# Performance work log

Hardware: AMD Instinct MI355X
Metric: run time of the kernel (lower is better)

Reference implementation:

```python
import jax, jax.numpy as jnp
import numpy as np

# dims (see shape_source): seq S = d_t+1 must equal d_k for the unary quantum loader
B, T, D_IN = 128, 127, 48
DK = 128
S = T + 1            # tokens incl. class token; S == DK
H, L = 8, 6
P = (S * S - S) // 2  # RBS angles per head (pyramid circuit over S wires)


def _pyramid_pairs(n):
    # deterministic pyramid ordering of n(n-1)/2 adjacent-pair Givens rotations
    a, b = [], []
    for k in range(n - 1):
        for i in range(k, -1, -1):
            a.append(i)
            b.append(i + 1)
    return np.asarray(a, np.int32), np.asarray(b, np.int32)


def _build_W(phi, pa, pb, n):
    # classical simulation of the RBS pyramid circuit restricted to the unary
    # subspace: product of Givens rotations -> orthogonal n x n matrix
    def step(W, inp):
        ia, ib, th = inp
        c, s = jnp.cos(th), jnp.sin(th)
        ra, rb = W[ia], W[ib]
        W = W.at[ia].set(c * ra - s * rb)
        W = W.at[ib].set(s * ra + c * rb)
        return W, None
    W0 = jnp.eye(n, dtype=phi.dtype)
    W, _ = jax.lax.scan(step, W0, (pa, pb, phi))
    return W


def _layer_norm(x, g, b, eps=1e-5):
    m = jnp.mean(x, axis=-1, keepdims=True)
    v = jnp.mean((x - m) ** 2, axis=-1, keepdims=True)
    return (x - m) * jax.lax.rsqrt(v + eps) * g + b


def setup_inputs() -> dict:
    key = jax.random.key(0)
    ks = jax.random.split(key, 8)
    f32 = jnp.float32
    return {
        "x": jax.random.normal(ks[0], (B, T, D_IN), f32),
        "embed_w": jax.random.normal(ks[1], (DK, D_IN), f32) / np.sqrt(D_IN),
        "embed_b": jnp.zeros((DK,), f32),
        "class_token": jax.random.normal(ks[2], (DK,), f32) / DK,
        "norm0_g": jnp.ones((DK,), f32),
        "norm0_b": jnp.zeros((DK,), f32),
        "Vw": jax.random.normal(ks[3], (L, H, DK, DK), f32) / np.sqrt(DK),
        "Vb": jnp.zeros((L, H, DK), f32),
        "ln_g": jnp.ones((L, H, DK), f32),
        "ln_b": jnp.zeros((L, H, DK), f32),
        "phi": jax.random.normal(ks[4], (L, H, P), f32) / np.sqrt(S),
        "merger_w": jax.random.normal(ks[5], (L, H), f32) / np.sqrt(H),
        "merger_b": jnp.zeros((L,), f32),
    }


def reference(x, embed_w, embed_b, class_token, norm0_g, norm0_b,
              Vw, Vb, ln_g, ln_b, phi, merger_w, merger_b):
    Bsz = x.shape[0]
    pa, pb = _pyramid_pairs(S)
    # orthogonal score matrices for every (layer, head)
    Ws = jax.vmap(lambda p: _build_W(p, pa, pb, S))(phi.reshape(L * H, P))
    Ws = Ws.reshape(L, H, S, S)

    # embed patches, prepend class token (pos_embedding add is a no-op in the
    # original source: bare `+self.pos_embedding` statement, so it is omitted)
    tok = jnp.einsum('btf,df->btd', x, embed_w) + embed_b
    h = jnp.concatenate([jnp.broadcast_to(class_token, (Bsz, 1, DK)), tok], axis=1)
    h = _layer_norm(h, norm0_g, norm0_b)

    scale = 1.0 / np.sqrt(DK)
    for l in range(L):
        nrm = jnp.sqrt(jnp.sum(h * h, axis=-1))      # input3: token norms [B,S]
        u = h / nrm[..., None]                        # unit tokens (convert_array)
        hh, nn, uu = h, nrm, u

        def head(W, vw, vb, g, be):
            V = jnp.einsum('bsd,ed->bse', hh, vw) + vb
            M = jnp.einsum('bsd,de,bte->bst', uu, W, uu)
            A = (M * M) * (nn[:, :, None] * nn[:, None, :])
            Pm = jax.nn.softmax(A * scale, axis=-1)
            return _layer_norm(jnp.einsum('bst,btd->bsd', Pm, V) + hh, g, be)

        hs = jax.vmap(head)(Ws[l], Vw[l], Vb[l], ln_g[l], ln_b[l])  # [H,B,S,D]
        h = jnp.einsum('hbsd,h->bsd', hs, merger_w[l]) + merger_b[l]
    return h[:, -1, :]
```

## Files before the change

### kernel.cpp

```cpp
#include <hip/hip_runtime.h>
#include <hip/hip_bf16.h>


typedef __bf16 bf16x8 __attribute__((ext_vector_type(8)));
typedef float  f32x4  __attribute__((ext_vector_type(4)));
typedef unsigned int u32;

__device__ __forceinline__ int sidx(int row, int col)
{
    return row * 128 + ((((col >> 3) ^ (row & 15)) << 3) | (col & 7));
}

__global__ void __launch_bounds__(256)
vw_frag_kernel(const float* __restrict__ vw, __bf16* __restrict__ cvwf)
{
    const int f    = blockIdx.x * 256 + threadIdx.x;
    const int lane = f & 63;
    const int k0   = (f >> 6) & 3;
    const int t    = (f >> 8) & 7;
    const int lh   = f >> 11;
    const int row  = t * 16 + (lane & 15);
    const int col  = k0 * 32 + (lane >> 4) * 8;

    const float* src = vw + (lh * 128 + row) * 128 + col;
    __bf16* dst = cvwf + f * 8;
#pragma unroll
    for (int j = 0; j < 8; j++) dst[j] = (__bf16)src[j];
}

__global__ void __launch_bounds__(64)
sincos_kernel(const float* __restrict__ phi, float2* __restrict__ csn)
{
    const int mat = blockIdx.x >> 8;
    const int t   = blockIdx.x & 255;
    const int j   = threadIdx.x;

    float th = 0.f;
    if (t < 253) {
        const int p = t & 1, i = 2 * j + p;
        const int lim = min(t, 252 - t);
        if (i <= lim) {
            const int k = (t + i) >> 1;
            th = phi[mat * 8128 + ((k * (k + 1)) >> 1) + (k - i)];
        }
    }
    float sn, cs;
    __sincosf(th, &sn, &cs);
    csn[(mat * 256 + t) * 64 + j] = make_float2(cs, sn);
}

__global__ void __launch_bounds__(64)
build_w_kernel(const float2* __restrict__ csn, __bf16* __restrict__ wt)
{
    const int mat = blockIdx.x >> 5;
    const int grp = blockIdx.x & 31;
    const int c0  = grp * 4;
    const int lam = threadIdx.x;

    const float2* base = csn + (mat * 256) * 64 + lam;

    float vlo[4], vhi[4];
#pragma unroll
    for (int j = 0; j < 4; j++) {
        vlo[j] = (2 * lam     == c0 + j) ? 1.f : 0.f;
        vhi[j] = (2 * lam + 1 == c0 + j) ? 1.f : 0.f;
    }

    float2 buf[3][16];
#pragma unroll
    for (int k = 0; k < 16; k++) buf[0][k] = base[k * 64];
#pragma unroll
    for (int k = 0; k < 16; k++) buf[1][k] = base[(16 + k) * 64];

#pragma unroll
    for (int g = 0; g < 16; g++) {
        const int cb = g % 3;
        if (g < 14) {
            const int nb = (g + 2) % 3;
#pragma unroll
            for (int k = 0; k < 16; k++)
                buf[nb][k] = base[((g + 2) * 16 + k) * 64];
        }
#pragma unroll
        for (int p = 0; p < 8; p++) {
            {
                const float cs = buf[cb][2 * p].x, sn = buf[cb][2 * p].y;
#pragma unroll
                for (int j = 0; j < 4; j++) {
                    float lo = vlo[j], hi = vhi[j];
                    vlo[j] = cs * lo - sn * hi;
                    vhi[j] = sn * lo + cs * hi;
                }
            }
            {
                const float cs = buf[cb][2 * p + 1].x, sn = buf[cb][2 * p + 1].y;
#pragma unroll
                for (int j = 0; j < 4; j++) {
                    float y  = __shfl_down(vlo[j], 1);
                    float x  = vhi[j];
                    float xn = cs * x - sn * y;
                    float yn = sn * x + cs * y;
                    vhi[j] = xn;
                    float z = __shfl_up(yn, 1);
                    if (lam > 0) vlo[j] = z;
                }
            }
        }
    }

    u32* wtu = (u32*)wt;
#pragma unroll
    for (int j = 0; j < 4; j++) {
        __bf16 va = (__bf16)vlo[j];
        __bf16 vb = (__bf16)vhi[j];
        u32 pk = (u32)__builtin_bit_cast(unsigned short, va)
               | ((u32)__builtin_bit_cast(unsigned short, vb) << 16);
        wtu[mat * 8192 + (c0 + j) * 64 + lam] = pk;
    }
}

static __device__ __forceinline__ float block_sum_128(float v, float* sred)
{
#pragma unroll
    for (int m = 32; m; m >>= 1) v += __shfl_xor(v, m);
    __syncthreads();
    if ((threadIdx.x & 63) == 0) sred[threadIdx.x >> 6] = v;
    __syncthreads();
    return sred[0] + sred[1];
}

__global__ void __launch_bounds__(128)
embed_kernel(const float* __restrict__ x,  const float* __restrict__ ew,
             const float* __restrict__ eb, const float* __restrict__ ct,
             const float* __restrict__ g0, const float* __restrict__ b0,
             float* __restrict__ hf, __bf16* __restrict__ hb, float* __restrict__ invn)
{
    __shared__ float sx[48];
    __shared__ float sred[2];
    const int b = blockIdx.x & 127, s = blockIdx.x >> 7, d = threadIdx.x;

    float val;
    if (s == 0) {
        val = ct[d];
    } else {
        if (d < 48) sx[d] = x[(b * 127 + (s - 1)) * 48 + d];
        __syncthreads();
        float aa = 0.f;
#pragma unroll
        for (int f = 0; f < 48; f++) aa = fmaf(sx[f], ew[d * 48 + f], aa);
        val = aa + eb[d];
    }
    float mean = block_sum_128(val, sred) * (1.f / 128.f);
    float xc   = val - mean;
    float var  = block_sum_128(xc * xc, sred) * (1.f / 128.f);
    float y    = xc * rsqrtf(var + 1e-5f) * g0[d] + b0[d];
    float ss   = block_sum_128(y * y, sred);

    const int o = (b * 128 + s) * 128 + d;
    hf[o] = y;
    hb[o] = (__bf16)y;
    if (d == 0) invn[b * 128 + s] = rsqrtf(ss);
}

__global__ void __launch_bounds__(512, 4)
attn_kernel(int l,
            const float*  __restrict__ hf,  const __bf16* __restrict__ hb,
            const float*  __restrict__ invn, const __bf16* __restrict__ wt,
            const __bf16* __restrict__ vwf, const float* __restrict__ vb,
            const float* __restrict__ lng,  const float* __restrict__ lnb,
            const float* __restrict__ mwp,  __bf16* __restrict__ hs)
{
    __shared__ __align__(16) __bf16 sH[128 * 128];
    __shared__ __align__(16) __bf16 sY[128 * 128];
    __shared__ float sInv[128];
    __shared__ float sVb[128];
    __shared__ float sLg[128];
    __shared__ float sLb[128];

    const int tid  = threadIdx.x;
    const int lane = tid & 63, w = tid >> 6;
    const int l15  = lane & 15, quad = lane >> 4;
    const int b    = blockIdx.x & 127;
    const int hh   = blockIdx.x >> 7;
    const int lh   = l * 8 + hh;

    const __bf16* hbp = hb + b * 16384;
    const __bf16* wtp = wt + lh * 16384;

#pragma unroll
    for (int c = 0; c < 4; c++) {
        int ch  = tid + c * 512;
        int row = ch >> 4, cc = ch & 15;
        bf16x8 hv = *(const bf16x8*)(hbp + ch * 8);
        bf16x8 wv = *(const bf16x8*)(wtp + ch * 8);
        *(bf16x8*)(&sH[sidx(row, cc * 8)]) = hv;
        *(bf16x8*)(&sY[sidx(row, cc * 8)]) = wv;
    }
    if (tid < 128) {
        sInv[tid] = invn[b * 128 + tid];
        sVb[tid]  = vb[lh * 128 + tid];
        sLg[tid]  = lng[lh * 128 + tid];
        sLb[tid]  = lnb[lh * 128 + tid];
    }
    __syncthreads();

    const int r0 = w * 16;
    const int kq = quad * 8;
    const int q4 = quad * 4;
    const f32x4 vzero = {0.f, 0.f, 0.f, 0.f};

    f32x4 acc[8];

    auto mmL = [&](const __bf16* Ab, const __bf16* Bb) {
#pragma unroll
        for (int t = 0; t < 8; t++) acc[t] = vzero;
#pragma unroll
        for (int k0 = 0; k0 < 128; k0 += 32) {
            const int kk = k0 + kq;
            bf16x8 a0 = *(const bf16x8*)(&Ab[sidx(r0 + l15, kk)]);
#pragma unroll
            for (int t = 0; t < 8; t++) {
                bf16x8 bb = *(const bf16x8*)(&Bb[sidx(t * 16 + l15, kk)]);
                acc[t] = __builtin_amdgcn_mfma_f32_16x16x32_bf16(a0, bb, acc[t], 0, 0, 0);
            }
        }
    };

    mmL(sH, sY);
    __syncthreads();
#pragma unroll
    for (int t = 0; t < 8; t++)
#pragma unroll
        for (int r = 0; r < 4; r++)
            sY[sidx(r0 + q4 + r, t * 16 + l15)] = (__bf16)acc[t][r];

    mmL(sY, sH);

    {
        const float scale2 = 0.08838834764831843f * 1.4426950408889634f;
        float invt[8];
#pragma unroll
        for (int t = 0; t < 8; t++) invt[t] = sInv[t * 16 + l15];
        float invs[4];
#pragma unroll
        for (int r = 0; r < 4; r++) invs[r] = sInv[r0 + q4 + r];

        float mx[4] = {-3e38f, -3e38f, -3e38f, -3e38f};
#pragma unroll
        for (int t = 0; t < 8; t++)
#pragma unroll
            for (int r = 0; r < 4; r++) {
                float g = acc[t][r];
                float v = g * g * invs[r] * invt[t] * scale2;
                acc[t][r] = v;
                mx[r] = fmaxf(mx[r], v);
            }
#pragma unroll
        for (int m = 1; m < 16; m <<= 1)
#pragma unroll
            for (int r = 0; r < 4; r++) mx[r] = fmaxf(mx[r], __shfl_xor(mx[r], m));

        float sm[4] = {0.f, 0.f, 0.f, 0.f};
#pragma unroll
        for (int t = 0; t < 8; t++)
#pragma unroll
            for (int r = 0; r < 4; r++) {
                float e = exp2f(acc[t][r] - mx[r]);
                acc[t][r] = e;
                sm[r] += e;
            }
#pragma unroll
        for (int m = 1; m < 16; m <<= 1)
#pragma unroll
            for (int r = 0; r < 4; r++) sm[r] += __shfl_xor(sm[r], m);
#pragma unroll
        for (int r = 0; r < 4; r++) sm[r] = 1.0f / sm[r];
#pragma unroll
        for (int t = 0; t < 8; t++)
#pragma unroll
            for (int r = 0; r < 4; r++)
                sY[sidx(r0 + q4 + r, t * 16 + l15)] = (__bf16)(acc[t][r] * sm[r]);
    }

    float hres[8][4];
    {
        const float* hfp = hf + (b * 128 + r0 + q4) * 128;
#pragma unroll
        for (int t = 0; t < 8; t++)
#pragma unroll
            for (int r = 0; r < 4; r++)
                hres[t][r] = hfp[r * 128 + t * 16 + l15];
    }

    {
        const __bf16* vbase = vwf + (size_t)lh * 16384;
#pragma unroll
        for (int t = 0; t < 8; t++) acc[t] = vzero;
#pragma unroll
        for (int k0c = 0; k0c < 4; k0c++) {
            const int kk = k0c * 32 + kq;
            bf16x8 a0 = *(const bf16x8*)(&sH[sidx(r0 + l15, kk)]);
#pragma unroll
            for (int t = 0; t < 8; t++) {
                bf16x8 bb = *(const bf16x8*)(vbase + ((t * 4 + k0c) * 64 + lane) * 8);
                acc[t] = __builtin_amdgcn_mfma_f32_16x16x32_bf16(a0, bb, acc[t], 0, 0, 0);
            }
        }
    }
    __syncthreads();

    {
        float vbv[8];
#pragma unroll
        for (int t = 0; t < 8; t++) vbv[t] = sVb[t * 16 + l15];
#pragma unroll
        for (int t = 0; t < 8; t++)
#pragma unroll
            for (int r = 0; r < 4; r++)
                sH[sidx(t * 16 + l15, r0 + q4 + r)] = (__bf16)(acc[t][r] + vbv[t]);
    }
    __syncthreads();

    mmL(sY, sH);

    {
        const float mw = mwp[lh];
        float lgv[8], lbv[8];
#pragma unroll
        for (int t = 0; t < 8; t++) {
            lgv[t] = sLg[t * 16 + l15];
            lbv[t] = sLb[t * 16 + l15];
        }
        float sum_[4] = {0.f, 0.f, 0.f, 0.f};
        float sq_[4]  = {0.f, 0.f, 0.f, 0.f};
#pragma unroll
        for (int t = 0; t < 8; t++)
#pragma unroll
            for (int r = 0; r < 4; r++) {
                float xx = acc[t][r] + hres[t][r];
                acc[t][r] = xx;
                sum_[r] += xx;
                sq_[r]  += xx * xx;
            }
#pragma unroll
        for (int m = 1; m < 16; m <<= 1)
#pragma unroll
            for (int r = 0; r < 4; r++) {
                sum_[r] += __shfl_xor(sum_[r], m);
                sq_[r]  += __shfl_xor(sq_[r], m);
            }
        float mean[4], rstd[4];
#pragma unroll
        for (int r = 0; r < 4; r++) {
            mean[r] = sum_[r] * (1.f / 128.f);
            float var = sq_[r] * (1.f / 128.f) - mean[r] * mean[r];
            rstd[r] = rsqrtf(fmaxf(var, 0.f) + 1e-5f);
        }
        __bf16* hsp = hs + ((hh * 128 + b) * 128 + r0 + q4) * 128;
#pragma unroll
        for (int t = 0; t < 8; t++)
#pragma unroll
            for (int r = 0; r < 4; r++) {
                float y = (acc[t][r] - mean[r]) * rstd[r] * lgv[t] + lbv[t];
                hsp[r * 128 + t * 16 + l15] = (__bf16)(y * mw);
            }
    }
}

__global__ void __launch_bounds__(128)
merge_kernel(const __bf16* __restrict__ hs, const float* __restrict__ mbp, int l,
             float* __restrict__ hf, __bf16* __restrict__ hb, float* __restrict__ invn,
             float* __restrict__ out, int last)
{
    __shared__ float sred[2];
    const int b = blockIdx.x & 127, s = blockIdx.x >> 7, d = threadIdx.x;

    float acc = mbp[l];
#pragma unroll
    for (int h = 0; h < 8; h++)
        acc += (float)hs[((h * 128 + b) * 128 + s) * 128 + d];

    float ss = block_sum_128(acc * acc, sred);

    const int o = (b * 128 + s) * 128 + d;
    hf[o] = acc;
    hb[o] = (__bf16)acc;
    if (d == 0) invn[b * 128 + s] = rsqrtf(ss);
    if (last && s == 127) out[b * 128 + d] = acc;
}

extern "C" void kernel_launch(void* const* d_in, const int* in_sizes, int n_in,
                              void* d_out, int out_size, void* d_ws, size_t ws_size,
                              hipStream_t stream)
{
    (void)in_sizes; (void)n_in; (void)out_size; (void)ws_size;

    const float* x   = (const float*)d_in[0];
    const float* ew  = (const float*)d_in[1];
    const float* eb  = (const float*)d_in[2];
    const float* ct  = (const float*)d_in[3];
    const float* g0  = (const float*)d_in[4];
    const float* b0  = (const float*)d_in[5];
    const float* vw  = (const float*)d_in[6];
    const float* vb  = (const float*)d_in[7];
    const float* lng = (const float*)d_in[8];
    const float* lnb = (const float*)d_in[9];
    const float* phi = (const float*)d_in[10];
    const float* mw  = (const float*)d_in[11];
    const float* mb  = (const float*)d_in[12];
    float* out = (float*)d_out;

    char* ws = (char*)d_ws;
    __bf16* wt   = (__bf16*)(ws);
    float*  hf   = (float*)(ws + 1572864);
    __bf16* hb   = (__bf16*)(ws + 9961472);
    float*  invn = (float*)(ws + 14155776);
    __bf16* hs   = (__bf16*)(ws + 14221312);
    __bf16* cvwf = (__bf16*)(ws + 47775744);
    float2* csn  = (float2*)(ws + 49348608);

    vw_frag_kernel<<<384, 256, 0, stream>>>(vw, cvwf);
    sincos_kernel<<<48 * 256, 64, 0, stream>>>(phi, csn);
    build_w_kernel<<<1536, 64, 0, stream>>>(csn, wt);
    embed_kernel<<<16384, 128, 0, stream>>>(x, ew, eb, ct, g0, b0, hf, hb, invn);
    for (int l = 0; l < 6; l++) {
        attn_kernel<<<1024, 512, 0, stream>>>(l, hf, hb, invn, wt, cvwf, vb,
                                              lng, lnb, mw, hs);
        merge_kernel<<<16384, 128, 0, stream>>>(hs, mb, l, hf, hb, invn, out,
                                                (l == 5) ? 1 : 0);
    }
}
```

Before: 427.1 us.

## Fuse head merge into next layer's attention load and merge prep kernels

Removes the separate merge kernel: each attention kernel now sums the 8 per-head outputs of the previous layer while loading its tile, and computes token norms in place, using ping-pong hs buffers. The sincos and Vw fragment prep kernels are merged into one launch, and the embed kernel handles 4 tokens per block and drops the norm output. This cuts launch count and the hf/hb write-then-read traffic per layer. In exchange, each of the 8 head blocks re-reads all 8 head slices, so there is redundant global reads (8x the merge read volume) and the residual is now taken from bf16 sums rather than fp32.

Result: slower. 709.2 us (+66.0%).

```diff
diff --git a/kernel.cpp b/kernel.cpp
--- a/kernel.cpp
+++ b/kernel.cpp
@@ -12,41 +12,38 @@
 }
 
 __global__ void __launch_bounds__(256)
-vw_frag_kernel(const float* __restrict__ vw, __bf16* __restrict__ cvwf)
-{
-    const int f    = blockIdx.x * 256 + threadIdx.x;
-    const int lane = f & 63;
-    const int k0   = (f >> 6) & 3;
-    const int t    = (f >> 8) & 7;
-    const int lh   = f >> 11;
-    const int row  = t * 16 + (lane & 15);
-    const int col  = k0 * 32 + (lane >> 4) * 8;
-
-    const float* src = vw + (lh * 128 + row) * 128 + col;
-    __bf16* dst = cvwf + f * 8;
-#pragma unroll
-    for (int j = 0; j < 8; j++) dst[j] = (__bf16)src[j];
-}
-
-__global__ void __launch_bounds__(64)
-sincos_kernel(const float* __restrict__ phi, float2* __restrict__ csn)
-{
-    const int mat = blockIdx.x >> 8;
-    const int t   = blockIdx.x & 255;
-    const int j   = threadIdx.x;
-
-    float th = 0.f;
-    if (t < 253) {
-        const int p = t & 1, i = 2 * j + p;
-        const int lim = min(t, 252 - t);
-        if (i <= lim) {
-            const int k = (t + i) >> 1;
-            th = phi[mat * 8128 + ((k * (k + 1)) >> 1) + (k - i)];
-        }
-    }
-    float sn, cs;
-    __sincosf(th, &sn, &cs);
-    csn[(mat * 256 + t) * 64 + j] = make_float2(cs, sn);
+prep_kernel(const float* __restrict__ phi, float2* __restrict__ csn,
+            const float* __restrict__ vw,  __bf16* __restrict__ cvwf)
+{
+    if (blockIdx.x < 3072) {
+        const int mat = blockIdx.x >> 6;
+        const int t   = ((blockIdx.x & 63) << 2) + (threadIdx.x >> 6);
+        const int j   = threadIdx.x & 63;
+        float th = 0.f;
+        if (t < 253) {
+            const int p = t & 1, i = 2 * j + p;
+            const int lim = min(t, 252 - t);
+            if (i <= lim) {
+                const int k = (t + i) >> 1;
+                th = phi[mat * 8128 + ((k * (k + 1)) >> 1) + (k - i)];
+            }
+        }
+        float sn, cs;
+        __sincosf(th, &sn, &cs);
+        csn[(mat * 256 + t) * 64 + j] = make_float2(cs, sn);
+    } else {
+        const int f    = (blockIdx.x - 3072) * 256 + threadIdx.x;
+        const int lane = f & 63;
+        const int k0   = (f >> 6) & 3;
+        const int t    = (f >> 8) & 7;
+        const int lh   = f >> 11;
+        const int row  = t * 16 + (lane & 15);
+        const int col  = k0 * 32 + (lane >> 4) * 8;
+        const float* src = vw + (lh * 128 + row) * 128 + col;
+        __bf16* dst = cvwf + f * 8;
+#pragma unroll
+        for (int j = 0; j < 8; j++) dst[j] = (__bf16)src[j];
+    }
 }
 
 __global__ void __launch_bounds__(64)
@@ -119,60 +116,63 @@
     }
 }
 
-static __device__ __forceinline__ float block_sum_128(float v, float* sred)
-{
-#pragma unroll
-    for (int m = 32; m; m >>= 1) v += __shfl_xor(v, m);
-    __syncthreads();
-    if ((threadIdx.x & 63) == 0) sred[threadIdx.x >> 6] = v;
-    __syncthreads();
-    return sred[0] + sred[1];
-}
-
-__global__ void __launch_bounds__(128)
+__global__ void __launch_bounds__(512)
 embed_kernel(const float* __restrict__ x,  const float* __restrict__ ew,
              const float* __restrict__ eb, const float* __restrict__ ct,
              const float* __restrict__ g0, const float* __restrict__ b0,
-             float* __restrict__ hf, __bf16* __restrict__ hb, float* __restrict__ invn)
-{
-    __shared__ float sx[48];
-    __shared__ float sred[2];
-    const int b = blockIdx.x & 127, s = blockIdx.x >> 7, d = threadIdx.x;
+             float* __restrict__ hf, __bf16* __restrict__ hb)
+{
+    __shared__ float sx[4][48];
+    __shared__ float sred[4][2];
+    const int d  = threadIdx.x & 127, sq = threadIdx.x >> 7;
+    const int wh = (threadIdx.x >> 6) & 1;
+    const int b  = blockIdx.x & 127;
+    const int s  = (blockIdx.x >> 7) * 4 + sq;
+
+    if (s > 0 && d < 48) sx[sq][d] = x[(b * 127 + (s - 1)) * 48 + d];
+    __syncthreads();
 
     float val;
     if (s == 0) {
         val = ct[d];
     } else {
-        if (d < 48) sx[d] = x[(b * 127 + (s - 1)) * 48 + d];
-        __syncthreads();
         float aa = 0.f;
 #pragma unroll
-        for (int f = 0; f < 48; f++) aa = fmaf(sx[f], ew[d * 48 + f], aa);
+        for (int f = 0; f < 48; f++) aa = fmaf(sx[sq][f], ew[d * 48 + f], aa);
         val = aa + eb[d];
     }
-    float mean = block_sum_128(val, sred) * (1.f / 128.f);
+    float v = val;
+#pragma unroll
+    for (int m = 32; m; m >>= 1) v += __shfl_xor(v, m);
+    if ((threadIdx.x & 63) == 0) sred[sq][wh] = v;
+    __syncthreads();
+    float mean = (sred[sq][0] + sred[sq][1]) * (1.f / 128.f);
     float xc   = val - mean;
-    float var  = block_sum_128(xc * xc, sred) * (1.f / 128.f);
-    float y    = xc * rsqrtf(var + 1e-5f) * g0[d] + b0[d];
-    float ss   = block_sum_128(y * y, sred);
+    __syncthreads();
+    v = xc * xc;
+#pragma unroll
+    for (int m = 32; m; m >>= 1) v += __shfl_xor(v, m);
+    if ((threadIdx.x & 63) == 0) sred[sq][wh] = v;
+    __syncthreads();
+    float var = (sred[sq][0] + sred[sq][1]) * (1.f / 128.f);
+    float y   = xc * rsqrtf(var + 1e-5f) * g0[d] + b0[d];
 
     const int o = (b * 128 + s) * 128 + d;
     hf[o] = y;
     hb[o] = (__bf16)y;
-    if (d == 0) invn[b * 128 + s] = rsqrtf(ss);
 }
 
 __global__ void __launch_bounds__(512, 4)
-attn_kernel(int l,
-            const float*  __restrict__ hf,  const __bf16* __restrict__ hb,
-            const float*  __restrict__ invn, const __bf16* __restrict__ wt,
-            const __bf16* __restrict__ vwf, const float* __restrict__ vb,
-            const float* __restrict__ lng,  const float* __restrict__ lnb,
-            const float* __restrict__ mwp,  __bf16* __restrict__ hs)
+attn_kernel(int l, int first,
+            const float*  __restrict__ hf,   const __bf16* __restrict__ hsrc,
+            const __bf16* __restrict__ wt,   const __bf16* __restrict__ vwf,
+            const float*  __restrict__ vb,   const float* __restrict__ lng,
+            const float*  __restrict__ lnb,  const float* __restrict__ mwp,
+            const float*  __restrict__ mbp,  __bf16* __restrict__ hs)
 {
     __shared__ __align__(16) __bf16 sH[128 * 128];
     __shared__ __align__(16) __bf16 sY[128 * 128];
-    __shared__ float sInv[128];
+    __shared__ float sInvR[128];
     __shared__ float sVb[128];
     __shared__ float sLg[128];
     __shared__ float sLb[128];
@@ -184,23 +184,44 @@
     const int hh   = blockIdx.x >> 7;
     const int lh   = l * 8 + hh;
 
-    const __bf16* hbp = hb + b * 16384;
     const __bf16* wtp = wt + lh * 16384;
+    const float mbv = first ? 0.f : mbp[l - 1];
 
 #pragma unroll
     for (int c = 0; c < 4; c++) {
         int ch  = tid + c * 512;
         int row = ch >> 4, cc = ch & 15;
-        bf16x8 hv = *(const bf16x8*)(hbp + ch * 8);
         bf16x8 wv = *(const bf16x8*)(wtp + ch * 8);
-        *(bf16x8*)(&sH[sidx(row, cc * 8)]) = hv;
+        float v[8];
+        if (first) {
+            bf16x8 hv = *(const bf16x8*)(hsrc + b * 16384 + ch * 8);
+#pragma unroll
+            for (int j = 0; j < 8; j++) v[j] = (float)hv[j];
+        } else {
+#pragma unroll
+            for (int j = 0; j < 8; j++) v[j] = mbv;
+#pragma unroll
+            for (int h8 = 0; h8 < 8; h8++) {
+                bf16x8 tv = *(const bf16x8*)(hsrc + (size_t)h8 * 2097152
+                                             + (b * 128 + row) * 128 + cc * 8);
+#pragma unroll
+                for (int j = 0; j < 8; j++) v[j] += (float)tv[j];
+            }
+        }
+        float ss = 0.f;
+        bf16x8 hv8;
+#pragma unroll
+        for (int j = 0; j < 8; j++) { ss = fmaf(v[j], v[j], ss); hv8[j] = (__bf16)v[j]; }
+        *(bf16x8*)(&sH[sidx(row, cc * 8)]) = hv8;
         *(bf16x8*)(&sY[sidx(row, cc * 8)]) = wv;
+#pragma unroll
+        for (int m = 1; m < 16; m <<= 1) ss += __shfl_xor(ss, m);
+        if ((tid & 15) == 0) sInvR[row] = ss;
     }
     if (tid < 128) {
-        sInv[tid] = invn[b * 128 + tid];
-        sVb[tid]  = vb[lh * 128 + tid];
-        sLg[tid]  = lng[lh * 128 + tid];
-        sLb[tid]  = lnb[lh * 128 + tid];
+        sVb[tid] = vb[lh * 128 + tid];
+        sLg[tid] = lng[lh * 128 + tid];
+        sLb[tid] = lnb[lh * 128 + tid];
     }
     __syncthreads();
 
@@ -240,10 +261,10 @@
         const float scale2 = 0.08838834764831843f * 1.4426950408889634f;
         float invt[8];
 #pragma unroll
-        for (int t = 0; t < 8; t++) invt[t] = sInv[t * 16 + l15];
+        for (int t = 0; t < 8; t++) invt[t] = rsqrtf(sInvR[t * 16 + l15]);
         float invs[4];
 #pragma unroll
-        for (int r = 0; r < 4; r++) invs[r] = sInv[r0 + q4 + r];
+        for (int r = 0; r < 4; r++) invs[r] = rsqrtf(sInvR[r0 + q4 + r]);
 
         float mx[4] = {-3e38f, -3e38f, -3e38f, -3e38f};
 #pragma unroll
@@ -283,13 +304,26 @@
     }
 
     float hres[8][4];
-    {
+    if (first) {
         const float* hfp = hf + (b * 128 + r0 + q4) * 128;
 #pragma unroll
         for (int t = 0; t < 8; t++)
 #pragma unroll
             for (int r = 0; r < 4; r++)
                 hres[t][r] = hfp[r * 128 + t * 16 + l15];
+    } else {
+#pragma unroll
+        for (int r = 0; r < 4; r++) {
+            const __bf16* hp = hsrc + (size_t)(b * 128 + r0 + q4 + r) * 128;
+#pragma unroll
+            for (int t = 0; t < 8; t++) {
+                float s = mbv;
+#pragma unroll
+                for (int h8 = 0; h8 < 8; h8++)
+                    s += (float)hp[(size_t)h8 * 2097152 + t * 16 + l15];
+                hres[t][r] = s;
+            }
+        }
     }
 
     {
@@ -368,25 +402,15 @@
 }
 
 __global__ void __launch_bounds__(128)
-merge_kernel(const __bf16* __restrict__ hs, const float* __restrict__ mbp, int l,
-             float* __restrict__ hf, __bf16* __restrict__ hb, float* __restrict__ invn,
-             float* __restrict__ out, int last)
-{
-    __shared__ float sred[2];
-    const int b = blockIdx.x & 127, s = blockIdx.x >> 7, d = threadIdx.x;
-
-    float acc = mbp[l];
-#pragma unroll
-    for (int h = 0; h < 8; h++)
-        acc += (float)hs[((h * 128 + b) * 128 + s) * 128 + d];
-
-    float ss = block_sum_128(acc * acc, sred);
-
-    const int o = (b * 128 + s) * 128 + d;
-    hf[o] = acc;
-    hb[o] = (__bf16)acc;
-    if (d == 0) invn[b * 128 + s] = rsqrtf(ss);
-    if (last && s == 127) out[b * 128 + d] = acc;
+finalize_kernel(const __bf16* __restrict__ hs5, const float* __restrict__ mbp,
+                float* __restrict__ out)
+{
+    const int b = blockIdx.x, d = threadIdx.x;
+    float acc = mbp[5];
+#pragma unroll
+    for (int h8 = 0; h8 < 8; h8++)
+        acc += (float)hs5[(size_t)h8 * 2097152 + (b * 128 + 127) * 128 + d];
+    out[b * 128 + d] = acc;
 }
 
 extern "C" void kernel_launch(void* const* d_in, const int* in_sizes, int n_in,
@@ -414,19 +438,21 @@
     __bf16* wt   = (__bf16*)(ws);
     float*  hf   = (float*)(ws + 1572864);
     __bf16* hb   = (__bf16*)(ws + 9961472);
-    float*  invn = (float*)(ws + 14155776);
-    __bf16* hs   = (__bf16*)(ws + 14221312);
-    __bf16* cvwf = (__bf16*)(ws + 47775744);
-    float2* csn  = (float2*)(ws + 49348608);
-
-    vw_frag_kernel<<<384, 256, 0, stream>>>(vw, cvwf);
-    sincos_kernel<<<48 * 256, 64, 0, stream>>>(phi, csn);
+    __bf16* hs0  = (__bf16*)(ws + 14155776);
+    __bf16* hs1  = (__bf16*)(ws + 47710208);
+    __bf16* cvwf = (__bf16*)(ws + 81264640);
+    float2* csn  = (float2*)(ws + 82837504);
+
+    prep_kernel<<<3456, 256, 0, stream>>>(phi, csn, vw, cvwf);
     build_w_kernel<<<1536, 64, 0, stream>>>(csn, wt);
-    embed_kernel<<<16384, 128, 0, stream>>>(x, ew, eb, ct, g0, b0, hf, hb, invn);
+    embed_kernel<<<4096, 512, 0, stream>>>(x, ew, eb, ct, g0, b0, hf, hb);
+
+    __bf16* hsbuf[2] = {hs0, hs1};
     for (int l = 0; l < 6; l++) {
-        attn_kernel<<<1024, 512, 0, stream>>>(l, hf, hb, invn, wt, cvwf, vb,
-                                              lng, lnb, mw, hs);
-        merge_kernel<<<16384, 128, 0, stream>>>(hs, mb, l, hf, hb, invn, out,
-                                                (l == 5) ? 1 : 0);
-    }
-}
+        const int first = (l == 0);
+        const __bf16* hsrc = first ? hb : hsbuf[(l & 1) ^ 1];
+        attn_kernel<<<1024, 512, 0, stream>>>(l, first, hf, hsrc, wt, cvwf,
+                                              vb, lng, lnb, mw, mb, hsbuf[l & 1]);
+    }
+    finalize_kernel<<<128, 128, 0, stream>>>(hsbuf[1], mb, out);
+}
```

## Store W in MFMA fragment layout and stream it from global; fuse prep kernels

Applied to the files above, without the earlier changes.

build_w now writes the rotation matrix directly in the per-lane MFMA B-fragment layout, so the first GEMM in attn_kernel reads W fragments from global/L2 instead of staging W through shared memory. This removes a shared-memory fill and one barrier per block. The sincos and Vw-fragment kernels are merged into one launch, and embed_kernel now handles four tokens per 512-thread block to cut launch and block overhead. In exchange, the first GEMM's operands come from global memory, which can add latency.

Result: slower. 463.4 us (+8.5%).

```diff
diff --git a/kernel.cpp b/kernel.cpp
--- a/kernel.cpp
+++ b/kernel.cpp
@@ -12,45 +12,42 @@
 }
 
 __global__ void __launch_bounds__(256)
-vw_frag_kernel(const float* __restrict__ vw, __bf16* __restrict__ cvwf)
-{
-    const int f    = blockIdx.x * 256 + threadIdx.x;
-    const int lane = f & 63;
-    const int k0   = (f >> 6) & 3;
-    const int t    = (f >> 8) & 7;
-    const int lh   = f >> 11;
-    const int row  = t * 16 + (lane & 15);
-    const int col  = k0 * 32 + (lane >> 4) * 8;
-
-    const float* src = vw + (lh * 128 + row) * 128 + col;
-    __bf16* dst = cvwf + f * 8;
-#pragma unroll
-    for (int j = 0; j < 8; j++) dst[j] = (__bf16)src[j];
+prep_kernel(const float* __restrict__ phi, float2* __restrict__ csn,
+            const float* __restrict__ vw,  __bf16* __restrict__ cvwf)
+{
+    if (blockIdx.x < 3072) {
+        const int mat = blockIdx.x >> 6;
+        const int t   = ((blockIdx.x & 63) << 2) + (threadIdx.x >> 6);
+        const int j   = threadIdx.x & 63;
+        float th = 0.f;
+        if (t < 253) {
+            const int p = t & 1, i = 2 * j + p;
+            const int lim = min(t, 252 - t);
+            if (i <= lim) {
+                const int k = (t + i) >> 1;
+                th = phi[mat * 8128 + ((k * (k + 1)) >> 1) + (k - i)];
+            }
+        }
+        float sn, cs;
+        __sincosf(th, &sn, &cs);
+        csn[(mat * 256 + t) * 64 + j] = make_float2(cs, sn);
+    } else {
+        const int f    = (blockIdx.x - 3072) * 256 + threadIdx.x;
+        const int lane = f & 63;
+        const int k0   = (f >> 6) & 3;
+        const int t    = (f >> 8) & 7;
+        const int lh   = f >> 11;
+        const int row  = t * 16 + (lane & 15);
+        const int col  = k0 * 32 + (lane >> 4) * 8;
+        const float* src = vw + (lh * 128 + row) * 128 + col;
+        __bf16* dst = cvwf + f * 8;
+#pragma unroll
+        for (int j = 0; j < 8; j++) dst[j] = (__bf16)src[j];
+    }
 }
 
 __global__ void __launch_bounds__(64)
-sincos_kernel(const float* __restrict__ phi, float2* __restrict__ csn)
-{
-    const int mat = blockIdx.x >> 8;
-    const int t   = blockIdx.x & 255;
-    const int j   = threadIdx.x;
-
-    float th = 0.f;
-    if (t < 253) {
-        const int p = t & 1, i = 2 * j + p;
-        const int lim = min(t, 252 - t);
-        if (i <= lim) {
-            const int k = (t + i) >> 1;
-            th = phi[mat * 8128 + ((k * (k + 1)) >> 1) + (k - i)];
-        }
-    }
-    float sn, cs;
-    __sincosf(th, &sn, &cs);
-    csn[(mat * 256 + t) * 64 + j] = make_float2(cs, sn);
-}
-
-__global__ void __launch_bounds__(64)
-build_w_kernel(const float2* __restrict__ csn, __bf16* __restrict__ wt)
+build_w_kernel(const float2* __restrict__ csn, __bf16* __restrict__ wtf)
 {
     const int mat = blockIdx.x >> 5;
     const int grp = blockIdx.x & 31;
@@ -108,53 +105,68 @@
         }
     }
 
-    u32* wtu = (u32*)wt;
+    u32* wtu = (u32*)wtf;
 #pragma unroll
     for (int j = 0; j < 4; j++) {
+        const int c = c0 + j;
         __bf16 va = (__bf16)vlo[j];
         __bf16 vb = (__bf16)vhi[j];
         u32 pk = (u32)__builtin_bit_cast(unsigned short, va)
                | ((u32)__builtin_bit_cast(unsigned short, vb) << 16);
-        wtu[mat * 8192 + (c0 + j) * 64 + lam] = pk;
-    }
-}
-
-static __device__ __forceinline__ float block_sum_128(float v, float* sred)
-{
-#pragma unroll
-    for (int m = 32; m; m >>= 1) v += __shfl_xor(v, m);
-    __syncthreads();
-    if ((threadIdx.x & 63) == 0) sred[threadIdx.x >> 6] = v;
-    __syncthreads();
-    return sred[0] + sred[1];
-}
-
-__global__ void __launch_bounds__(128)
+        const int idx = (((c >> 4) * 4 + (lam >> 4)) * 64
+                         + ((lam >> 2) & 3) * 16 + (c & 15)) * 4 + (lam & 3);
+        wtu[mat * 8192 + idx] = pk;
+    }
+}
+
+__global__ void __launch_bounds__(512)
 embed_kernel(const float* __restrict__ x,  const float* __restrict__ ew,
              const float* __restrict__ eb, const float* __restrict__ ct,
              const float* __restrict__ g0, const float* __restrict__ b0,
-             float* __restrict__ hf, __bf16* __restrict__ hb, float* __restrict__ invn)
-{
-    __shared__ float sx[48];
-    __shared__ float sred[2];
-    const int b = blockIdx.x & 127, s = blockIdx.x >> 7, d = threadIdx.x;
+             float* __restrict__ hf, __bf16* __restrict__ hb,
+             float* __restrict__ invn)
+{
+    __shared__ float sx[4][48];
+    __shared__ float sred[4][2];
+    const int d  = threadIdx.x & 127, sq = threadIdx.x >> 7;
+    const int wh = (threadIdx.x >> 6) & 1;
+    const int b  = blockIdx.x & 127;
+    const int s  = (blockIdx.x >> 7) * 4 + sq;
+
+    if (s > 0 && d < 48) sx[sq][d] = x[(b * 127 + (s - 1)) * 48 + d];
+    __syncthreads();
 
     float val;
     if (s == 0) {
         val = ct[d];
     } else {
-        if (d < 48) sx[d] = x[(b * 127 + (s - 1)) * 48 + d];
-        __syncthreads();
         float aa = 0.f;
 #pragma unroll
-        for (int f = 0; f < 48; f++) aa = fmaf(sx[f], ew[d * 48 + f], aa);
+        for (int f = 0; f < 48; f++) aa = fmaf(sx[sq][f], ew[d * 48 + f], aa);
         val = aa + eb[d];
     }
-    float mean = block_sum_128(val, sred) * (1.f / 128.f);
+    float v = val;
+#pragma unroll
+    for (int m = 32; m; m >>= 1) v += __shfl_xor(v, m);
+    if ((threadIdx.x & 63) == 0) sred[sq][wh] = v;
+    __syncthreads();
+    float mean = (sred[sq][0] + sred[sq][1]) * (1.f / 128.f);
     float xc   = val - mean;
-    float var  = block_sum_128(xc * xc, sred) * (1.f / 128.f);
-    float y    = xc * rsqrtf(var + 1e-5f) * g0[d] + b0[d];
-    float ss   = block_sum_128(y * y, sred);
+    __syncthreads();
+    v = xc * xc;
+#pragma unroll
+    for (int m = 32; m; m >>= 1) v += __shfl_xor(v, m);
+    if ((threadIdx.x & 63) == 0) sred[sq][wh] = v;
+    __syncthreads();
+    float var = (sred[sq][0] + sred[sq][1]) * (1.f / 128.f);
+    float y   = xc * rsqrtf(var + 1e-5f) * g0[d] + b0[d];
+    __syncthreads();
+    v = y * y;
+#pragma unroll
+    for (int m = 32; m; m >>= 1) v += __shfl_xor(v, m);
+    if ((threadIdx.x & 63) == 0) sred[sq][wh] = v;
+    __syncthreads();
+    float ss = sred[sq][0] + sred[sq][1];
 
     const int o = (b * 128 + s) * 128 + d;
     hf[o] = y;
@@ -165,7 +177,7 @@
 __global__ void __launch_bounds__(512, 4)
 attn_kernel(int l,
             const float*  __restrict__ hf,  const __bf16* __restrict__ hb,
-            const float*  __restrict__ invn, const __bf16* __restrict__ wt,
+            const float*  __restrict__ invn, const __bf16* __restrict__ wtf,
             const __bf16* __restrict__ vwf, const float* __restrict__ vb,
             const float* __restrict__ lng,  const float* __restrict__ lnb,
             const float* __restrict__ mwp,  __bf16* __restrict__ hs)
@@ -185,16 +197,13 @@
     const int lh   = l * 8 + hh;
 
     const __bf16* hbp = hb + b * 16384;
-    const __bf16* wtp = wt + lh * 16384;
 
 #pragma unroll
     for (int c = 0; c < 4; c++) {
         int ch  = tid + c * 512;
         int row = ch >> 4, cc = ch & 15;
         bf16x8 hv = *(const bf16x8*)(hbp + ch * 8);
-        bf16x8 wv = *(const bf16x8*)(wtp + ch * 8);
         *(bf16x8*)(&sH[sidx(row, cc * 8)]) = hv;
-        *(bf16x8*)(&sY[sidx(row, cc * 8)]) = wv;
     }
     if (tid < 128) {
         sInv[tid] = invn[b * 128 + tid];
@@ -211,30 +220,43 @@
 
     f32x4 acc[8];
 
-    auto mmL = [&](const __bf16* Ab, const __bf16* Bb) {
+    auto mmG = [&](const __bf16* gbase) {
+#pragma unroll
+        for (int t = 0; t < 8; t++) acc[t] = vzero;
+        const __bf16* gp = gbase + lane * 8;
+#pragma unroll
+        for (int k0c = 0; k0c < 4; k0c++) {
+            bf16x8 a0 = *(const bf16x8*)(&sH[sidx(r0 + l15, k0c * 32 + kq)]);
+#pragma unroll
+            for (int t = 0; t < 8; t++) {
+                bf16x8 bb = *(const bf16x8*)(gp + (t * 4 + k0c) * 512);
+                acc[t] = __builtin_amdgcn_mfma_f32_16x16x32_bf16(a0, bb, acc[t], 0, 0, 0);
+            }
+        }
+    };
+    auto mmL = [&]() {
 #pragma unroll
         for (int t = 0; t < 8; t++) acc[t] = vzero;
 #pragma unroll
         for (int k0 = 0; k0 < 128; k0 += 32) {
             const int kk = k0 + kq;
-            bf16x8 a0 = *(const bf16x8*)(&Ab[sidx(r0 + l15, kk)]);
+            bf16x8 a0 = *(const bf16x8*)(&sY[sidx(r0 + l15, kk)]);
 #pragma unroll
             for (int t = 0; t < 8; t++) {
-                bf16x8 bb = *(const bf16x8*)(&Bb[sidx(t * 16 + l15, kk)]);
+                bf16x8 bb = *(const bf16x8*)(&sH[sidx(t * 16 + l15, kk)]);
                 acc[t] = __builtin_amdgcn_mfma_f32_16x16x32_bf16(a0, bb, acc[t], 0, 0, 0);
             }
         }
     };
 
-    mmL(sH, sY);
-    __syncthreads();
+    mmG(wtf + (size_t)lh * 16384);
 #pragma unroll
     for (int t = 0; t < 8; t++)
 #pragma unroll
         for (int r = 0; r < 4; r++)
             sY[sidx(r0 + q4 + r, t * 16 + l15)] = (__bf16)acc[t][r];
 
-    mmL(sY, sH);
+    mmL();
 
     {
         const float scale2 = 0.08838834764831843f * 1.4426950408889634f;
@@ -292,21 +314,7 @@
                 hres[t][r] = hfp[r * 128 + t * 16 + l15];
     }
 
-    {
-        const __bf16* vbase = vwf + (size_t)lh * 16384;
-#pragma unroll
-        for (int t = 0; t < 8; t++) acc[t] = vzero;
-#pragma unroll
-        for (int k0c = 0; k0c < 4; k0c++) {
-            const int kk = k0c * 32 + kq;
-            bf16x8 a0 = *(const bf16x8*)(&sH[sidx(r0 + l15, kk)]);
-#pragma unroll
-            for (int t = 0; t < 8; t++) {
-                bf16x8 bb = *(const bf16x8*)(vbase + ((t * 4 + k0c) * 64 + lane) * 8);
-                acc[t] = __builtin_amdgcn_mfma_f32_16x16x32_bf16(a0, bb, acc[t], 0, 0, 0);
-            }
-        }
-    }
+    mmG(vwf + (size_t)lh * 16384);
     __syncthreads();
 
     {
@@ -321,7 +329,7 @@
     }
     __syncthreads();
 
-    mmL(sY, sH);
+    mmL();
 
     {
         const float mw = mwp[lh];
@@ -365,6 +373,16 @@
                 hsp[r * 128 + t * 16 + l15] = (__bf16)(y * mw);
             }
     }
+}
+
+static __device__ __forceinline__ float block_sum_128(float v, float* sred)
+{
+#pragma unroll
+    for (int m = 32; m; m >>= 1) v += __shfl_xor(v, m);
+    __syncthreads();
+    if ((threadIdx.x & 63) == 0) sred[threadIdx.x >> 6] = v;
+    __syncthreads();
+    return sred[0] + sred[1];
 }
 
 __global__ void __launch_bounds__(128)
@@ -411,7 +429,7 @@
     float* out = (float*)d_out;
 
     char* ws = (char*)d_ws;
-    __bf16* wt   = (__bf16*)(ws);
+    __bf16* wtf  = (__bf16*)(ws);
     float*  hf   = (float*)(ws + 1572864);
     __bf16* hb   = (__bf16*)(ws + 9961472);
     float*  invn = (float*)(ws + 14155776);
@@ -419,12 +437,11 @@
     __bf16* cvwf = (__bf16*)(ws + 47775744);
     float2* csn  = (float2*)(ws + 49348608);
 
-    vw_frag_kernel<<<384, 256, 0, stream>>>(vw, cvwf);
-    sincos_kernel<<<48 * 256, 64, 0, stream>>>(phi, csn);
-    build_w_kernel<<<1536, 64, 0, stream>>>(csn, wt);
-    embed_kernel<<<16384, 128, 0, stream>>>(x, ew, eb, ct, g0, b0, hf, hb, invn);
+    prep_kernel<<<3456, 256, 0, stream>>>(phi, csn, vw, cvwf);
+    build_w_kernel<<<1536, 64, 0, stream>>>(csn, wtf);
+    embed_kernel<<<4096, 512, 0, stream>>>(x, ew, eb, ct, g0, b0, hf, hb, invn);
     for (int l = 0; l < 6; l++) {
-        attn_kernel<<<1024, 512, 0, stream>>>(l, hf, hb, invn, wt, cvwf, vb,
+        attn_kernel<<<1024, 512, 0, stream>>>(l, hf, hb, invn, wtf, cvwf, vb,
                                               lng, lnb, mw, hs);
         merge_kernel<<<16384, 128, 0, stream>>>(hs, mb, l, hf, hb, invn, out,
                                                 (l == 5) ? 1 : 0);
```
